# Optimization experiments

Measured on AMD Instinct MI355X. Metric: run time of the kernel, lower is better.

## Reference

```python
import jax, jax.numpy as jnp
from jax import lax
import numpy as np


def _fps(xyz, M):
    # Farthest point sampling: sequential over M steps, vectorized over batch.
    B, N, _ = xyz.shape
    def body(carry, _):
        dists, far = carry                       # dists:[B,N], far:[B]
        c = xyz[jnp.arange(B), far]              # [B,3] current centroid
        d = jnp.sum((xyz - c[:, None, :]) ** 2, axis=-1)
        dists = jnp.minimum(dists, d)
        nxt = jnp.argmax(dists, axis=-1).astype(jnp.int32)
        return (dists, nxt), far
    init = (jnp.full((B, N), 1e10, xyz.dtype), jnp.zeros((B,), jnp.int32))
    _, inds = lax.scan(body, init, None, length=M)
    return inds.T                                # [B, M]


def _ball_query(xyz, new_xyz, radius, K):
    # For each centroid pick first K point indices within radius; pad with first hit.
    N = xyz.shape[1]
    d2 = jnp.sum((new_xyz[:, :, None, :] - xyz[:, None, :, :]) ** 2, axis=-1)  # [B,M,N]
    ids = jnp.where(d2 <= radius * radius, jnp.arange(N)[None, None, :], N)
    ids = jnp.sort(ids, axis=-1)[..., :K]        # [B,M,K]
    return jnp.where(ids == N, ids[..., :1], ids)


_gather = jax.vmap(lambda p, i: p[i])            # p:[N,C], i:[M,K] -> [M,K,C]


def _mlp(x, layers):
    # Shared per-point MLP (1x1 conv + ReLU chain); BN omitted as in source head.
    for w, b in layers:
        x = jax.nn.relu(jnp.einsum('bmkc,cd->bmkd', x, w) + b)
    return x


def _sa(xyz, points, M, radius, K, layers):
    # Set-abstraction: FPS -> ball query -> group (centered xyz ++ feats) -> MLP -> max over K.
    fi = _fps(xyz, M)                                        # [B,M]
    new_xyz = jnp.take_along_axis(xyz, fi[..., None], axis=1)  # [B,M,3]
    gi = _ball_query(xyz, new_xyz, radius, K)                # [B,M,K]
    g_xyz = _gather(xyz, gi) - new_xyz[:, :, None, :]        # [B,M,K,3]
    g = jnp.concatenate([g_xyz, _gather(points, gi)], axis=-1)
    return new_xyz, jnp.max(_mlp(g, layers), axis=2)         # [B,M,Cout]


def _forward(xyz, points,
             w1a, b1a, w1b, b1b, w1c, b1c,
             w2a, b2a, w2b, b2b, w2c, b2c,
             w3a, b3a, w3b, b3b, w3c, b3c,
             lin1_w, lin2_w, cls_w, cls_b):
    B = xyz.shape[0]
    x1, f1 = _sa(xyz, points, 512, 0.2, 32, [(w1a, b1a), (w1b, b1b), (w1c, b1c)])
    x2, f2 = _sa(x1, f1, 128, 0.4, 64, [(w2a, b2a), (w2b, b2b), (w2c, b2c)])
    # group_all: single group containing all 128 points, feats = [xyz ++ points] (259 ch)
    g = jnp.concatenate([x2, f2], axis=-1)[:, None]           # [B,1,128,259]
    f3 = jnp.max(_mlp(g, [(w3a, b3a), (w3b, b3b), (w3c, b3c)]), axis=2)  # [B,1,1024]
    net = f3.reshape(B, -1)
    net = jax.nn.relu(net @ lin1_w)   # linear1 (no bias) + ReLU; dropout=identity (eval)
    net = jax.nn.relu(net @ lin2_w)
    return net @ cls_w + cls_b


def setup_inputs() -> dict:
    key = jax.random.key(0)
    ks = iter(jax.random.split(key, 40))
    B, N, NC = 32, 1024, 40
    inp = {}
    inp['xyz'] = jax.random.uniform(next(ks), (B, N, 3), jnp.float32, -1.0, 1.0)
    inp['points'] = jax.random.normal(next(ks), (B, N, 3), jnp.float32)
    def lin(cin, cout):
        w = jax.random.normal(next(ks), (cin, cout), jnp.float32) / np.float32(np.sqrt(cin))
        return w, jnp.zeros((cout,), jnp.float32)
    dims = {'1': [(6, 64), (64, 64), (64, 128)],
            '2': [(131, 128), (128, 128), (128, 256)],
            '3': [(259, 256), (256, 512), (512, 1024)]}
    for s, layer_dims in dims.items():
        for tag, (ci, co) in zip('abc', layer_dims):
            w, b = lin(ci, co)
            inp['w%s%s' % (s, tag)] = w
            inp['b%s%s' % (s, tag)] = b
    inp['lin1_w'] = jax.random.normal(next(ks), (1024, 512), jnp.float32) / np.float32(32.0)
    inp['lin2_w'] = jax.random.normal(next(ks), (512, 256), jnp.float32) / np.float32(np.sqrt(512))
    inp['cls_w'] = jax.random.normal(next(ks), (256, NC), jnp.float32) / np.float32(16.0)
    inp['cls_b'] = jnp.zeros((NC,), jnp.float32)
    return inp


def reference(xyz, points,
              w1a, b1a, w1b, b1b, w1c, b1c,
              w2a, b2a, w2b, b2b, w2c, b2c,
              w3a, b3a, w3b, b3b, w3c, b3c,
              lin1_w, lin2_w, cls_w, cls_b):
    return _forward(xyz, points,
                    w1a, b1a, w1b, b1b, w1c, b1c,
                    w2a, b2a, w2b, b2b, w2c, b2c,
                    w3a, b3a, w3b, b3b, w3c, b3c,
                    lin1_w, lin2_w, cls_w, cls_b)
```

## Files before the change

kernel.cpp:

```cpp
#include <hip/hip_runtime.h>

#define DEVFN __device__ __forceinline__

static inline int ceil_div(int a, int b) { return (a + b - 1) / b; }

typedef __attribute__((ext_vector_type(8))) short         bf16x8;
typedef __attribute__((ext_vector_type(4))) float         f32x4;
typedef __attribute__((ext_vector_type(8))) unsigned short u16x8;
typedef unsigned short us;

DEVFN us f2bf(float x) {
    unsigned u = __float_as_uint(x);
    unsigned r = ((u >> 16) & 1u) + 0x7fffu;
    return (us)((u + r) >> 16);
}
DEVFN float bf2f(us h) { return __uint_as_float(((unsigned)h) << 16); }

template<int CTRL>
DEVFN double dpp_max_step(double v)
{
    int lo = __double2loint(v), hi = __double2hiint(v);
    int tlo = __builtin_amdgcn_update_dpp(lo, lo, CTRL, 0xF, 0xF, false);
    int thi = __builtin_amdgcn_update_dpp(hi, hi, CTRL, 0xF, 0xF, false);
    return fmax(v, __hiloint2double(thi, tlo));
}

template<int N>
__global__ __launch_bounds__(64) void fps_kernel(const float* __restrict__ xyz, int M,
                                                 int* __restrict__ out_idx,
                                                 float* __restrict__ nxout)
{
    constexpr int PPL = N / 64;
    int b = blockIdx.x, lane = threadIdx.x;
    __shared__ float4 sp[N];
    const float* p = xyz + (size_t)b * N * 3;
    float px[PPL], py[PPL], pz[PPL], dd[PPL];
    unsigned lo[PPL];
    #pragma unroll
    for (int j = 0; j < PPL; ++j) {
        int idx = lane + 64 * j;
        px[j] = p[idx*3+0]; py[j] = p[idx*3+1]; pz[j] = p[idx*3+2];
        sp[idx] = make_float4(px[j], py[j], pz[j], 0.f);
        dd[j] = 1e10f;
        lo[j] = ~(unsigned)idx;
    }
    __syncthreads();
    int far = 0;
    for (int s = 0; s < M; ++s) {
        float4 c4 = sp[far];
        if (lane == 0) {
            out_idx[(size_t)b*M + s] = far;
            nxout[((size_t)b*M + s)*3 + 0] = c4.x;
            nxout[((size_t)b*M + s)*3 + 1] = c4.y;
            nxout[((size_t)b*M + s)*3 + 2] = c4.z;
        }
        double cand[PPL];
        #pragma unroll
        for (int j = 0; j < PPL; ++j) {
            float dx = __fsub_rn(px[j], c4.x);
            float dy = __fsub_rn(py[j], c4.y);
            float dz = __fsub_rn(pz[j], c4.z);
            float d  = __fadd_rn(__fadd_rn(__fmul_rn(dx,dx), __fmul_rn(dy,dy)),
                                 __fmul_rn(dz,dz));
            float nd = fminf(dd[j], d);
            dd[j] = nd;
            cand[j] = __hiloint2double(__float_as_int(nd), (int)lo[j]);
        }
        #pragma unroll
        for (int st = PPL/2; st > 0; st >>= 1)
            #pragma unroll
            for (int j = 0; j < PPL; ++j)
                if (j < st) cand[j] = fmax(cand[j], cand[j + st]);
        double v = cand[0];
        v = dpp_max_step<0xB1>(v);
        v = dpp_max_step<0x4E>(v);
        v = dpp_max_step<0x124>(v);
        v = dpp_max_step<0x128>(v);
        v = dpp_max_step<0x142>(v);
        v = dpp_max_step<0x143>(v);
        int wlo = __builtin_amdgcn_readlane(__double2loint(v), 63);
        far = (int)(~(unsigned)wlo);
    }
}

__global__ void ballquery_kernel(const float* __restrict__ xyz,
                                 const float* __restrict__ new_xyz,
                                 int* __restrict__ gi,
                                 int B, int N, int M, int K, float r2)
{
    int t = blockIdx.x * blockDim.x + threadIdx.x;
    if (t >= B * M) return;
    int b = t / M;
    const float* p = xyz + (size_t)b * N * 3;
    float cx = new_xyz[t*3+0], cy = new_xyz[t*3+1], cz = new_xyz[t*3+2];
    int* out = gi + (size_t)t * K;
    int cnt = 0, first = 0;
    bool havefirst = false;
    for (int i = 0; i < N; ++i) {
        float dx = __fsub_rn(p[i*3+0], cx);
        float dy = __fsub_rn(p[i*3+1], cy);
        float dz = __fsub_rn(p[i*3+2], cz);
        float d  = __fadd_rn(__fadd_rn(__fmul_rn(dx,dx), __fmul_rn(dy,dy)),
                             __fmul_rn(dz,dz));
        if (d <= r2) {
            if (!havefirst) { first = i; havefirst = true; }
            out[cnt++] = i;
            if (cnt == K) break;
        }
    }
    for (; cnt < K; ++cnt) out[cnt] = first;
}

DEVFN float f4_elem(const float4& v, int u) {
    return u == 0 ? v.x : u == 1 ? v.y : u == 2 ? v.z : v.w;
}

__global__ void wsplit_kernel(const float* __restrict__ w,
                              us* __restrict__ wh, us* __restrict__ wl,
                              int CItot, int CO, int CIpad, int ro)
{
    int t = blockIdx.x * 256 + threadIdx.x;
    if (t >= CIpad * CO) return;
    int co = t / CIpad, ci = t % CIpad;
    int src = ci + ro;
    float v = (src < CItot) ? w[(size_t)src * CO + co] : 0.f;
    us h = f2bf(v);
    wh[t] = h;
    wl[t] = f2bf(v - bf2f(h));
}

__global__ __launch_bounds__(256) void sa1_l1_fps2_kernel(
    const float* __restrict__ xyz, const float* __restrict__ feats,
    const float* __restrict__ new_xyz , const int* __restrict__ gi,
    const float* __restrict__ w, const float* __restrict__ bias,
    us* __restrict__ oh, us* __restrict__ ol,
    int row0, int nb_main, int fps_on,
    int* __restrict__ fps2, float* __restrict__ nx2)
{
    __shared__ float4 sp[512];
    if ((int)blockIdx.x >= nb_main) {
        if (!fps_on) return;
        constexpr int N = 512, PPL = 8, MS = 128;
        const int b   = blockIdx.x - nb_main;
        const int tid = threadIdx.x, lane = tid & 63;
        float px[PPL], py[PPL], pz[PPL], dd[PPL];
        unsigned lo[PPL];
        if (tid < 64) {
            const float* p = new_xyz + (size_t)b * N * 3;
            #pragma unroll
            for (int j = 0; j < PPL; ++j) {
                int idx = lane + 64 * j;
                px[j] = p[idx*3+0]; py[j] = p[idx*3+1]; pz[j] = p[idx*3+2];
                sp[idx] = make_float4(px[j], py[j], pz[j], 0.f);
                dd[j] = 1e10f;
                lo[j] = ~(unsigned)idx;
            }
        }
        __syncthreads();
        if (tid >= 64) return;
        int far = 0;
        for (int s = 0; s < MS; ++s) {
            float4 c4 = sp[far];
            if (lane == 0) {
                fps2[(size_t)b*MS + s] = far;
                nx2[((size_t)b*MS + s)*3 + 0] = c4.x;
                nx2[((size_t)b*MS + s)*3 + 1] = c4.y;
                nx2[((size_t)b*MS + s)*3 + 2] = c4.z;
            }
            double cand[PPL];
            #pragma unroll
            for (int j = 0; j < PPL; ++j) {
                float dx = __fsub_rn(px[j], c4.x);
                float dy = __fsub_rn(py[j], c4.y);
                float dz = __fsub_rn(pz[j], c4.z);
                float d  = __fadd_rn(__fadd_rn(__fmul_rn(dx,dx), __fmul_rn(dy,dy)),
                                     __fmul_rn(dz,dz));
                float nd = fminf(dd[j], d);
                dd[j] = nd;
                cand[j] = __hiloint2double(__float_as_int(nd), (int)lo[j]);
            }
            #pragma unroll
            for (int st = PPL/2; st > 0; st >>= 1)
                #pragma unroll
                for (int j = 0; j < PPL; ++j)
                    if (j < st) cand[j] = fmax(cand[j], cand[j + st]);
            double v = cand[0];
            v = dpp_max_step<0xB1>(v);
            v = dpp_max_step<0x4E>(v);
            v = dpp_max_step<0x124>(v);
            v = dpp_max_step<0x128>(v);
            v = dpp_max_step<0x142>(v);
            v = dpp_max_step<0x143>(v);
            int wlo = __builtin_amdgcn_readlane(__double2loint(v), 63);
            far = (int)(~(unsigned)wlo);
        }
        return;
    }
    constexpr int CF = 3, CO = 64, KPTS = 32, N = 1024, M = 512, WCH = 16;
    const int lane = threadIdx.x & 63;
    const int wv   = __builtin_amdgcn_readfirstlane(threadIdx.x >> 6);
    const int rl   = blockIdx.x * 64 + lane;
    const int row  = row0 + rl;
    const int cent = row / KPTS;
    const int b    = cent / M;
    const int idx  = gi[row];
    const float* pp  = xyz + ((size_t)b*N + idx)*3;
    const float* cc3 = new_xyz + (size_t)cent*3;
    float a0 = __fsub_rn(pp[0], cc3[0]);
    float a1 = __fsub_rn(pp[1], cc3[1]);
    float a2 = __fsub_rn(pp[2], cc3[2]);
    const float* frow = feats + ((size_t)b*N + idx)*CF;
    float f0 = frow[0], f1v = frow[1], f2v = frow[2];
    const float* wcol = w + wv*WCH;
    const float* bcol = bias + wv*WCH;
    float acc[WCH];
    #pragma unroll
    for (int j = 0; j < WCH; ++j) {
        float a = bcol[j];
        a += a0 * wcol[0*CO + j];
        a += a1 * wcol[1*CO + j];
        a += a2 * wcol[2*CO + j];
        a += f0 * wcol[3*CO + j];
        a += f1v * wcol[4*CO + j];
        a += f2v * wcol[5*CO + j];
        acc[j] = a;
    }
    #pragma unroll
    for (int j8 = 0; j8 < WCH; j8 += 8) {
        u16x8 hv, lv;
        #pragma unroll
        for (int u = 0; u < 8; ++u) {
            float v = fmaxf(acc[j8+u], 0.f);
            us h = f2bf(v);
            hv[u] = h;
            lv[u] = f2bf(v - bf2f(h));
        }
        size_t o = (size_t)rl*CO + wv*WCH + j8;
        *(u16x8*)(&oh[o]) = hv;
        *(u16x8*)(&ol[o]) = lv;
    }
}

__global__ __launch_bounds__(256) void sa1_l2_bq2_kernel(
    const us* __restrict__ ah, const us* __restrict__ al,
    const us* __restrict__ wh, const us* __restrict__ wl,
    const float* __restrict__ bias,
    us* __restrict__ oh, us* __restrict__ ol,
    int nb_main, int bq_on,
    const float* __restrict__ nx1, const float* __restrict__ nx2,
    int* __restrict__ gi2)
{
    if ((int)blockIdx.x >= nb_main) {
        if (!bq_on) return;
        int t = (blockIdx.x - nb_main) * 256 + threadIdx.x;
        if (t >= 32 * 128) return;
        constexpr int N = 512, M = 128, K = 64;
        const float r2 = (float)(0.4*0.4);
        int b = t / M;
        const float* p = nx1 + (size_t)b * N * 3;
        float cx = nx2[t*3+0], cy = nx2[t*3+1], cz = nx2[t*3+2];
        int* out = gi2 + (size_t)t * K;
        int cnt = 0, first = 0;
        bool havefirst = false;
        for (int i = 0; i < N; ++i) {
            float dx = __fsub_rn(p[i*3+0], cx);
            float dy = __fsub_rn(p[i*3+1], cy);
            float dz = __fsub_rn(p[i*3+2], cz);
            float d  = __fadd_rn(__fadd_rn(__fmul_rn(dx,dx), __fmul_rn(dy,dy)),
                                 __fmul_rn(dz,dz));
            if (d <= r2) {
                if (!havefirst) { first = i; havefirst = true; }
                out[cnt++] = i;
                if (cnt == K) break;
            }
        }
        for (; cnt < K; ++cnt) out[cnt] = first;
        return;
    }
    constexpr int CI = 64, CO = 64, KT = 2, NTILE = 4, MROW = 4;
    const int wid  = threadIdx.x >> 6;
    const int lane = threadIdx.x & 63;
    const int m    = lane & 15;
    const int kg   = lane >> 4;
    const int blockrow = blockIdx.x * (64 * MROW);
    bf16x8 Ahf[MROW * KT], Alf[MROW * KT];
    #pragma unroll
    for (int t = 0; t < MROW; ++t) {
        const us* arh = ah + (size_t)(blockrow + t*64 + wid*16 + m) * CI + kg * 8;
        const us* arl = al + (size_t)(blockrow + t*64 + wid*16 + m) * CI + kg * 8;
        #pragma unroll
        for (int kt = 0; kt < KT; ++kt) {
            Ahf[t*KT + kt] = *(const bf16x8*)(arh + kt*32);
            Alf[t*KT + kt] = *(const bf16x8*)(arl + kt*32);
        }
    }
    #pragma unroll
    for (int nt = 0; nt < NTILE; ++nt) {
        f32x4 acc[MROW];
        #pragma unroll
        for (int t = 0; t < MROW; ++t) acc[t] = (f32x4){0.f, 0.f, 0.f, 0.f};
        const us* wbh = wh + (size_t)(nt*16 + m) * CI + kg * 8;
        const us* wbl = wl + (size_t)(nt*16 + m) * CI + kg * 8;
        #pragma unroll
        for (int kt = 0; kt < KT; ++kt) {
            bf16x8 Bh = *(const bf16x8*)(wbh + kt*32);
            bf16x8 Bl = *(const bf16x8*)(wbl + kt*32);
            #pragma unroll
            for (int t = 0; t < MROW; ++t) {
                acc[t] = __builtin_amdgcn_mfma_f32_16x16x32_bf16(Ahf[t*KT+kt], Bh, acc[t], 0, 0, 0);
                acc[t] = __builtin_amdgcn_mfma_f32_16x16x32_bf16(Ahf[t*KT+kt], Bl, acc[t], 0, 0, 0);
                acc[t] = __builtin_amdgcn_mfma_f32_16x16x32_bf16(Alf[t*KT+kt], Bh, acc[t], 0, 0, 0);
            }
        }
        int dcol = nt*16 + m;
        float bv = bias[dcol];
        #pragma unroll
        for (int t = 0; t < MROW; ++t)
            #pragma unroll
            for (int r = 0; r < 4; ++r) {
                float v = fmaxf(acc[t][r] + bv, 0.f);
                size_t o = (size_t)(blockrow + t*64 + wid*16 + kg*4 + r) * CO + dcol;
                us h = f2bf(v);
                oh[o] = h;
                ol[o] = f2bf(v - bf2f(h));
            }
    }
}

template<int CI, int CO, int NTILE, int MROW, int KPTS, int OUTMODE>
__global__ __launch_bounds__(256) void mfma_layer_kernel(
    const us* __restrict__ ah, const us* __restrict__ al,
    const us* __restrict__ wh, const us* __restrict__ wl,
    const float* __restrict__ bias,
    us* __restrict__ oh, us* __restrict__ ol,
    float* __restrict__ ofp, int rowbase)
{
    constexpr int KT = CI / 32;
    static_assert(KT * MROW <= 18, "A-preload register budget");
    __shared__ float partial[4][OUTMODE >= 2 ? MROW : 1][OUTMODE >= 2 ? 16*NTILE : 1];
    const int wid  = threadIdx.x >> 6;
    const int lane = threadIdx.x & 63;
    const int m    = lane & 15;
    const int kg   = lane >> 4;
    const int blockrow = blockIdx.x * (64 * MROW);
    const int colbase  = blockIdx.y * (16 * NTILE);
    bf16x8 Ahf[MROW * KT], Alf[MROW * KT];
    #pragma unroll
    for (int t = 0; t < MROW; ++t) {
        const us* arh = ah + (size_t)(blockrow + t*64 + wid*16 + m) * CI + kg * 8;
        const us* arl = al + (size_t)(blockrow + t*64 + wid*16 + m) * CI + kg * 8;
        #pragma unroll
        for (int kt = 0; kt < KT; ++kt) {
            Ahf[t*KT + kt] = *(const bf16x8*)(arh + kt*32);
            Alf[t*KT + kt] = *(const bf16x8*)(arl + kt*32);
        }
    }
    #pragma unroll
    for (int nt = 0; nt < NTILE; ++nt) {
        f32x4 acc[MROW];
        #pragma unroll
        for (int t = 0; t < MROW; ++t) acc[t] = (f32x4){0.f, 0.f, 0.f, 0.f};
        const us* wbh = wh + (size_t)(colbase + nt*16 + m) * CI + kg * 8;
        const us* wbl = wl + (size_t)(colbase + nt*16 + m) * CI + kg * 8;
        #pragma unroll
        for (int kt = 0; kt < KT; ++kt) {
            bf16x8 Bh = *(const bf16x8*)(wbh + kt*32);
            bf16x8 Bl = *(const bf16x8*)(wbl + kt*32);
            #pragma unroll
            for (int t = 0; t < MROW; ++t) {
                acc[t] = __builtin_amdgcn_mfma_f32_16x16x32_bf16(Ahf[t*KT+kt], Bh, acc[t], 0, 0, 0);
                acc[t] = __builtin_amdgcn_mfma_f32_16x16x32_bf16(Ahf[t*KT+kt], Bl, acc[t], 0, 0, 0);
                acc[t] = __builtin_amdgcn_mfma_f32_16x16x32_bf16(Alf[t*KT+kt], Bh, acc[t], 0, 0, 0);
            }
        }
        int dcol = colbase + nt*16 + m;
        float bv = bias[dcol];
        #pragma unroll
        for (int t = 0; t < MROW; ++t) {
            float v[4];
            #pragma unroll
            for (int r = 0; r < 4; ++r) v[r] = fmaxf(acc[t][r] + bv, 0.f);
            if constexpr (OUTMODE == 0) {
                #pragma unroll
                for (int r = 0; r < 4; ++r) {
                    size_t o = (size_t)(blockrow + t*64 + wid*16 + kg*4 + r) * CO + dcol;
                    us h = f2bf(v[r]);
                    oh[o] = h;
                    ol[o] = f2bf(v[r] - bf2f(h));
                }
            } else if constexpr (OUTMODE == 1) {
                #pragma unroll
                for (int r = 0; r < 4; ++r)
                    ofp[(size_t)(blockrow + t*64 + wid*16 + kg*4 + r) * CO + dcol] = v[r];
            } else {
                float mx = fmaxf(fmaxf(v[0], v[1]), fmaxf(v[2], v[3]));
                mx = fmaxf(mx, __shfl_xor(mx, 16));
                mx = fmaxf(mx, __shfl_xor(mx, 32));
                if (lane < 16) partial[wid][t][nt*16 + m] = mx;
            }
        }
    }
    if constexpr (OUTMODE >= 2) {
        __syncthreads();
        for (int c = threadIdx.x; c < 16*NTILE; c += 256) {
            #pragma unroll
            for (int t = 0; t < MROW; ++t) {
                if constexpr (KPTS == 64) {
                    float mx = fmaxf(fmaxf(partial[0][t][c], partial[1][t][c]),
                                     fmaxf(partial[2][t][c], partial[3][t][c]));
                    int cent = (rowbase + blockrow) / 64 + t;
                    if constexpr (OUTMODE == 2) {
                        ofp[(size_t)cent*CO + colbase + c] = mx;
                    } else {
                        size_t o = (size_t)cent*CO + colbase + c;
                        us h = f2bf(mx);
                        oh[o] = h; ol[o] = f2bf(mx - bf2f(h));
                    }
                } else {
                    int cent0 = (rowbase + blockrow) / 32 + t*2;
                    float v0 = fmaxf(partial[0][t][c], partial[1][t][c]);
                    float v1 = fmaxf(partial[2][t][c], partial[3][t][c]);
                    if constexpr (OUTMODE == 2) {
                        ofp[(size_t)cent0*CO + colbase + c]     = v0;
                        ofp[(size_t)(cent0+1)*CO + colbase + c] = v1;
                    } else {
                        size_t o0 = (size_t)cent0*CO + colbase + c;
                        size_t o1 = (size_t)(cent0+1)*CO + colbase + c;
                        us h0 = f2bf(v0), h1 = f2bf(v1);
                        oh[o0] = h0; ol[o0] = f2bf(v0 - bf2f(h0));
                        oh[o1] = h1; ol[o1] = f2bf(v1 - bf2f(h1));
                    }
                }
            }
        }
    }
}

template<int NTILE, int MROW>
__global__ __launch_bounds__(256) void mfma_sa2l1_kernel(
    const float* __restrict__ sxyz, const float* __restrict__ cxyz,
    const int* __restrict__ gi,
    const us* __restrict__ f1h, const us* __restrict__ f1l,
    const float* __restrict__ w,
    const us* __restrict__ wh, const us* __restrict__ wl,
    const float* __restrict__ bias,
    us* __restrict__ oh, us* __restrict__ ol,
    int rowbase)
{
    constexpr int CI = 128, CO = 128, KT = 4, KPTS = 64, M = 128, N = 512;
    const int wid  = threadIdx.x >> 6;
    const int lane = threadIdx.x & 63;
    const int m    = lane & 15;
    const int kg   = lane >> 4;
    const int blockrow = blockIdx.x * (64 * MROW);
    const int colbase  = blockIdx.y * (16 * NTILE);
    bf16x8 Ahf[MROW * KT], Alf[MROW * KT];
    #pragma unroll
    for (int t = 0; t < MROW; ++t) {
        int grow = rowbase + blockrow + t*64 + wid*16 + m;
        int cent = grow / KPTS;
        int b    = cent / M;
        int idx  = gi[grow];
        const us* arh = f1h + ((size_t)b*N + idx) * CI + kg * 8;
        const us* arl = f1l + ((size_t)b*N + idx) * CI + kg * 8;
        #pragma unroll
        for (int kt = 0; kt < KT; ++kt) {
            Ahf[t*KT + kt] = *(const bf16x8*)(arh + kt*32);
            Alf[t*KT + kt] = *(const bf16x8*)(arl + kt*32);
        }
    }
    float dx[MROW][4], dy[MROW][4], dz[MROW][4];
    #pragma unroll
    for (int t = 0; t < MROW; ++t)
        #pragma unroll
        for (int r = 0; r < 4; ++r) {
            int grow = rowbase + blockrow + t*64 + wid*16 + kg*4 + r;
            int cent = grow / KPTS;
            int b    = cent / M;
            int idx  = gi[grow];
            const float* pp = sxyz + ((size_t)b*N + idx)*3;
            const float* cc = cxyz + (size_t)cent*3;
            dx[t][r] = __fsub_rn(pp[0], cc[0]);
            dy[t][r] = __fsub_rn(pp[1], cc[1]);
            dz[t][r] = __fsub_rn(pp[2], cc[2]);
        }
    #pragma unroll
    for (int nt = 0; nt < NTILE; ++nt) {
        f32x4 acc[MROW];
        #pragma unroll
        for (int t = 0; t < MROW; ++t) acc[t] = (f32x4){0.f, 0.f, 0.f, 0.f};
        const us* wbh = wh + (size_t)(colbase + nt*16 + m) * CI + kg * 8;
        const us* wbl = wl + (size_t)(colbase + nt*16 + m) * CI + kg * 8;
        #pragma unroll
        for (int kt = 0; kt < KT; ++kt) {
            bf16x8 Bh = *(const bf16x8*)(wbh + kt*32);
            bf16x8 Bl = *(const bf16x8*)(wbl + kt*32);
            #pragma unroll
            for (int t = 0; t < MROW; ++t) {
                acc[t] = __builtin_amdgcn_mfma_f32_16x16x32_bf16(Ahf[t*KT+kt], Bh, acc[t], 0, 0, 0);
                acc[t] = __builtin_amdgcn_mfma_f32_16x16x32_bf16(Ahf[t*KT+kt], Bl, acc[t], 0, 0, 0);
                acc[t] = __builtin_amdgcn_mfma_f32_16x16x32_bf16(Alf[t*KT+kt], Bh, acc[t], 0, 0, 0);
            }
        }
        int dcol = colbase + nt*16 + m;
        float w0 = w[0*CO + dcol], w1 = w[1*CO + dcol], w2 = w[2*CO + dcol];
        float bv = bias[dcol];
        #pragma unroll
        for (int t = 0; t < MROW; ++t)
            #pragma unroll
            for (int r = 0; r < 4; ++r) {
                float v = acc[t][r] + bv + dx[t][r]*w0 + dy[t][r]*w1 + dz[t][r]*w2;
                v = fmaxf(v, 0.f);
                size_t o = (size_t)(blockrow + t*64 + wid*16 + kg*4 + r) * CO + dcol;
                us h = f2bf(v);
                oh[o] = h;
                ol[o] = f2bf(v - bf2f(h));
            }
    }
}

__global__ void concat_split_kernel(const float* __restrict__ a, const float* __restrict__ f,
                                    us* __restrict__ oh, us* __restrict__ ol,
                                    int R, int CF, int CIpad)
{
    int t = blockIdx.x * 256 + threadIdx.x;
    if (t >= R * CIpad) return;
    int r = t / CIpad, c = t % CIpad;
    float v;
    if (c < 3) v = a[r*3 + c];
    else if (c < CF + 3) v = f[(size_t)r * CF + (c - 3)];
    else v = 0.f;
    us h = f2bf(v);
    oh[t] = h;
    ol[t] = f2bf(v - bf2f(h));
}

template<int RELU, int HASB>
__global__ __launch_bounds__(256) void fc_kernel(
    const float* __restrict__ A, const float* __restrict__ W,
    const float* __restrict__ bias, float* __restrict__ Cc,
    int Mr, int Nc, int Kd)
{
    int t = blockIdx.x * 256 + threadIdx.x;
    if (t >= Mr * Nc) return;
    int row = t / Nc, col = t % Nc;
    const float* a = A + (size_t)row * Kd;
    const float* w = W + col;
    float acc = 0.f;
    #pragma unroll 8
    for (int k = 0; k < Kd; ++k)
        acc += a[k] * w[(size_t)k * Nc];
    if (HASB) acc += bias[col];
    if (RELU) acc = fmaxf(acc, 0.f);
    Cc[t] = acc;
}

__global__ void rowmax_kernel(const float* __restrict__ in, float* __restrict__ out,
                              int B, int P, int C)
{
    int t = blockIdx.x * blockDim.x + threadIdx.x;
    if (t >= B * C) return;
    int b = t / C, c = t % C;
    const float* p = in + (size_t)b * P * C + c;
    float mx = p[0];
    for (int i = 1; i < P; ++i) mx = fmaxf(mx, p[(size_t)i * C]);
    out[t] = mx;
}

extern "C" void kernel_launch(void* const* d_in, const int* in_sizes, int n_in,
                              void* d_out, int out_size, void* d_ws, size_t ws_size,
                              hipStream_t stream)
{
    const float* xyz    = (const float*)d_in[0];
    const float* points = (const float*)d_in[1];
    const float* w1a = (const float*)d_in[2];  const float* b1a = (const float*)d_in[3];
    const float* w1b = (const float*)d_in[4];  const float* b1b = (const float*)d_in[5];
    const float* w1c = (const float*)d_in[6];  const float* b1c = (const float*)d_in[7];
    const float* w2a = (const float*)d_in[8];  const float* b2a = (const float*)d_in[9];
    const float* w2b = (const float*)d_in[10]; const float* b2b = (const float*)d_in[11];
    const float* w2c = (const float*)d_in[12]; const float* b2c = (const float*)d_in[13];
    const float* w3a = (const float*)d_in[14]; const float* b3a = (const float*)d_in[15];
    const float* w3b = (const float*)d_in[16]; const float* b3b = (const float*)d_in[17];
    const float* w3c = (const float*)d_in[18]; const float* b3c = (const float*)d_in[19];
    const float* lin1 = (const float*)d_in[20];
    const float* lin2 = (const float*)d_in[21];
    const float* clsw = (const float*)d_in[22];
    const float* clsb = (const float*)d_in[23];

    char* ws = (char*)d_ws;
    size_t off = 0;
    auto alloc = [&](size_t bytes) -> void* {
        void* p = ws + off;
        off += (bytes + 255) & ~(size_t)255;
        return p;
    };
    int*   fps1 = (int*)  alloc((size_t)32*512*4);
    float* nx1  = (float*)alloc((size_t)32*512*3*4);
    int*   gi1  = (int*)  alloc((size_t)32*512*32*4);
    int*   fps2 = (int*)  alloc((size_t)32*128*4);
    float* nx2  = (float*)alloc((size_t)32*128*3*4);
    int*   gi2  = (int*)  alloc((size_t)32*128*64*4);
    float* f2   = (float*)alloc((size_t)32*128*256*4);
    float* h3c  = (float*)alloc((size_t)4096*1024*4);
    float* f3   = (float*)alloc((size_t)32*1024*4);
    float* fc1  = (float*)alloc((size_t)32*512*4);
    float* fc2  = (float*)alloc((size_t)32*256*4);

    us* w1bh = (us*)alloc(64*64*2);     us* w1bl = (us*)alloc(64*64*2);
    us* w1ch = (us*)alloc(128*64*2);    us* w1cl = (us*)alloc(128*64*2);
    us* w2ah = (us*)alloc(128*128*2);   us* w2al = (us*)alloc(128*128*2);
    us* w2bh = (us*)alloc(128*128*2);   us* w2bl = (us*)alloc(128*128*2);
    us* w2ch = (us*)alloc(256*128*2);   us* w2cl = (us*)alloc(256*128*2);
    us* w3ah = (us*)alloc(256*288*2);   us* w3al = (us*)alloc(256*288*2);
    us* w3bh = (us*)alloc(512*256*2);   us* w3bl = (us*)alloc(512*256*2);
    us* w3ch = (us*)alloc(1024*512*2);  us* w3cl = (us*)alloc(1024*512*2);
    us* f1h  = (us*)alloc((size_t)16384*128*2);
    us* f1l  = (us*)alloc((size_t)16384*128*2);
    us* g3H  = (us*)alloc((size_t)4096*288*2);  us* g3L  = (us*)alloc((size_t)4096*288*2);
    us* h3aH = (us*)alloc((size_t)4096*256*2);  us* h3aL = (us*)alloc((size_t)4096*256*2);
    us* h3bH = (us*)alloc((size_t)4096*512*2);  us* h3bL = (us*)alloc((size_t)4096*512*2);

    size_t avail = (ws_size > off + 1024) ? (ws_size - off - 1024) : 0;
    size_t bufcap = avail / 4;
    if (bufcap > (size_t)67200000) bufcap = 67200000;
    us* Ah = (us*)alloc(bufcap); us* Al = (us*)alloc(bufcap);
    us* Bh = (us*)alloc(bufcap); us* Bl = (us*)alloc(bufcap);

    auto wsp = [&](const float* w, int CItot, int CO, int CIpad, int ro, us* wh, us* wl) {
        wsplit_kernel<<<ceil_div(CIpad*CO, 256), 256, 0, stream>>>(w, wh, wl, CItot, CO, CIpad, ro);
    };
    wsp(w1b, 64, 64, 64, 0,   w1bh, w1bl);
    wsp(w1c, 64, 128, 64, 0,  w1ch, w1cl);
    wsp(w2a, 131, 128, 128, 3, w2ah, w2al);
    wsp(w2b, 128, 128, 128, 0, w2bh, w2bl);
    wsp(w2c, 128, 256, 128, 0, w2ch, w2cl);
    wsp(w3a, 259, 256, 288, 0, w3ah, w3al);
    wsp(w3b, 256, 512, 256, 0, w3bh, w3bl);
    wsp(w3c, 512, 1024, 512, 0, w3ch, w3cl);

    fps_kernel<1024><<<32, 64, 0, stream>>>(xyz, 512, fps1, nx1);
    ballquery_kernel<<<ceil_div(32*512, 256), 256, 0, stream>>>(
        xyz, nx1, gi1, 32, 1024, 512, 32, (float)(0.2*0.2));
    {
        const int rows = 32*512*32;
        int ch = (int)((bufcap / (64*2)) & ~(size_t)1023);
        if (ch > rows) ch = rows;
        if (ch < 1024) ch = 1024;
        int first = 1;
        for (int r0 = 0; r0 < rows; r0 += ch) {
            int rc = rows - r0 < ch ? rows - r0 : ch;
            int nb1 = rc/64, nb2 = rc/256;
            sa1_l1_fps2_kernel<<<nb1 + (first ? 32 : 0), 256, 0, stream>>>(
                xyz, points, nx1, gi1, w1a, b1a, Ah, Al, r0, nb1, first, fps2, nx2);
            sa1_l2_bq2_kernel<<<nb2 + (first ? 16 : 0), 256, 0, stream>>>(
                Ah, Al, w1bh, w1bl, b1b, Bh, Bl, nb2, first, nx1, nx2, gi2);
            mfma_layer_kernel<64, 128, 8, 4, 32, 3><<<dim3(nb2, 1), 256, 0, stream>>>(
                Bh, Bl, w1ch, w1cl, b1c, f1h, f1l, nullptr, r0);
            first = 0;
        }
    }

    {
        const int rows = 32*128*64;
        int ch = (int)((bufcap / (128*2)) & ~(size_t)1023);
        if (ch > rows) ch = rows;
        if (ch < 1024) ch = 1024;
        for (int r0 = 0; r0 < rows; r0 += ch) {
            int rc = rows - r0 < ch ? rows - r0 : ch;
            mfma_sa2l1_kernel<8, 2><<<dim3(rc/128, 1), 256, 0, stream>>>(
                nx1, nx2, gi2, f1h, f1l, w2a, w2ah, w2al, b2a, Ah, Al, r0);
            mfma_layer_kernel<128, 128, 8, 4, 0, 0><<<dim3(rc/256, 1), 256, 0, stream>>>(
                Ah, Al, w2bh, w2bl, b2b, Bh, Bl, nullptr, 0);
            mfma_layer_kernel<128, 256, 16, 4, 64, 2><<<dim3(rc/256, 1), 256, 0, stream>>>(
                Bh, Bl, w2ch, w2cl, b2c, nullptr, nullptr, f2, r0);
        }
    }

    concat_split_kernel<<<ceil_div(4096*288, 256), 256, 0, stream>>>(
        nx2, f2, g3H, g3L, 4096, 256, 288);
    mfma_layer_kernel<288, 256, 2, 1, 0, 0><<<dim3(4096/64, 256/32), 256, 0, stream>>>(
        g3H, g3L, w3ah, w3al, b3a, h3aH, h3aL, nullptr, 0);
    mfma_layer_kernel<256, 512, 2, 2, 0, 0><<<dim3(4096/128, 512/32), 256, 0, stream>>>(
        h3aH, h3aL, w3bh, w3bl, b3b, h3bH, h3bL, nullptr, 0);
    mfma_layer_kernel<512, 1024, 4, 1, 0, 1><<<dim3(4096/64, 1024/64), 256, 0, stream>>>(
        h3bH, h3bL, w3ch, w3cl, b3c, nullptr, nullptr, h3c, 0);
    rowmax_kernel<<<ceil_div(32*1024, 256), 256, 0, stream>>>(h3c, f3, 32, 128, 1024);

    fc_kernel<1,0><<<ceil_div(32*512, 256), 256, 0, stream>>>(
        f3, lin1, nullptr, fc1, 32, 512, 1024);
    fc_kernel<1,0><<<ceil_div(32*256, 256), 256, 0, stream>>>(
        fc1, lin2, nullptr, fc2, 32, 256, 512);
    fc_kernel<0,1><<<ceil_div(32*40, 256), 256, 0, stream>>>(
        fc2, clsw, clsb, (float*)d_out, 32, 40, 256);
}
```

Before: 1.253 ms.

## Split farthest point sampling across four waves with LDS cross-wave argmax

The FPS loops now run on a 256-thread block instead of a single 64-lane wave, so each lane holds a quarter as many points. After the intra-wave DPP max, each wave writes its candidate to a double-buffered LDS slot and a block barrier lets all threads combine the four candidates. This cuts the per-step serial arithmetic on the latency-bound FPS chain, but adds a barrier and LDS round trip to every step. The second-stage FPS embedded in the fused kernel uses the same shared body.

```diff
diff --git a/kernel.cpp b/kernel.cpp
--- a/kernel.cpp
+++ b/kernel.cpp
@@ -26,19 +26,17 @@
 }
 
 template<int N>
-__global__ __launch_bounds__(64) void fps_kernel(const float* __restrict__ xyz, int M,
-                                                 int* __restrict__ out_idx,
-                                                 float* __restrict__ nxout)
-{
-    constexpr int PPL = N / 64;
-    int b = blockIdx.x, lane = threadIdx.x;
-    __shared__ float4 sp[N];
-    const float* p = xyz + (size_t)b * N * 3;
+DEVFN void fps4_body(const float* __restrict__ p, int MS,
+                     int* __restrict__ oidx, float* __restrict__ onx,
+                     float4* sp, double* kslots)
+{
+    constexpr int PPL = N / 256;
+    const int tid = threadIdx.x;
     float px[PPL], py[PPL], pz[PPL], dd[PPL];
     unsigned lo[PPL];
     #pragma unroll
     for (int j = 0; j < PPL; ++j) {
-        int idx = lane + 64 * j;
+        int idx = tid + 256 * j;
         px[j] = p[idx*3+0]; py[j] = p[idx*3+1]; pz[j] = p[idx*3+2];
         sp[idx] = make_float4(px[j], py[j], pz[j], 0.f);
         dd[j] = 1e10f;
@@ -46,13 +44,11 @@
     }
     __syncthreads();
     int far = 0;
-    for (int s = 0; s < M; ++s) {
+    for (int s = 0; s < MS; ++s) {
         float4 c4 = sp[far];
-        if (lane == 0) {
-            out_idx[(size_t)b*M + s] = far;
-            nxout[((size_t)b*M + s)*3 + 0] = c4.x;
-            nxout[((size_t)b*M + s)*3 + 1] = c4.y;
-            nxout[((size_t)b*M + s)*3 + 2] = c4.z;
+        if (tid == 0) {
+            oidx[s] = far;
+            onx[s*3+0] = c4.x; onx[s*3+1] = c4.y; onx[s*3+2] = c4.z;
         }
         double cand[PPL];
         #pragma unroll
@@ -78,9 +74,24 @@
         v = dpp_max_step<0x128>(v);
         v = dpp_max_step<0x142>(v);
         v = dpp_max_step<0x143>(v);
-        int wlo = __builtin_amdgcn_readlane(__double2loint(v), 63);
-        far = (int)(~(unsigned)wlo);
-    }
+        if ((tid & 63) == 63) kslots[(s & 1)*4 + (tid >> 6)] = v;
+        __syncthreads();
+        const double* ks = kslots + (s & 1)*4;
+        double kx = fmax(fmax(ks[0], ks[1]), fmax(ks[2], ks[3]));
+        far = (int)(~(unsigned)__double2loint(kx));
+    }
+}
+
+template<int N>
+__global__ __launch_bounds__(256) void fps4_kernel(const float* __restrict__ xyz, int M,
+                                                   int* __restrict__ out_idx,
+                                                   float* __restrict__ nxout)
+{
+    __shared__ float4 sp[N];
+    __shared__ double kslots[8];
+    int b = blockIdx.x;
+    fps4_body<N>(xyz + (size_t)b * N * 3, M,
+                 out_idx + (size_t)b * M, nxout + (size_t)b * M * 3, sp, kslots);
 }
 
 __global__ void ballquery_kernel(const float* __restrict__ xyz,
@@ -138,62 +149,13 @@
     int* __restrict__ fps2, float* __restrict__ nx2)
 {
     __shared__ float4 sp[512];
+    __shared__ double kslots[8];
     if ((int)blockIdx.x >= nb_main) {
         if (!fps_on) return;
-        constexpr int N = 512, PPL = 8, MS = 128;
-        const int b   = blockIdx.x - nb_main;
-        const int tid = threadIdx.x, lane = tid & 63;
-        float px[PPL], py[PPL], pz[PPL], dd[PPL];
-        unsigned lo[PPL];
-        if (tid < 64) {
-            const float* p = new_xyz + (size_t)b * N * 3;
-            #pragma unroll
-            for (int j = 0; j < PPL; ++j) {
-                int idx = lane + 64 * j;
-                px[j] = p[idx*3+0]; py[j] = p[idx*3+1]; pz[j] = p[idx*3+2];
-                sp[idx] = make_float4(px[j], py[j], pz[j], 0.f);
-                dd[j] = 1e10f;
-                lo[j] = ~(unsigned)idx;
-            }
-        }
-        __syncthreads();
-        if (tid >= 64) return;
-        int far = 0;
-        for (int s = 0; s < MS; ++s) {
-            float4 c4 = sp[far];
-            if (lane == 0) {
-                fps2[(size_t)b*MS + s] = far;
-                nx2[((size_t)b*MS + s)*3 + 0] = c4.x;
-                nx2[((size_t)b*MS + s)*3 + 1] = c4.y;
-                nx2[((size_t)b*MS + s)*3 + 2] = c4.z;
-            }
-            double cand[PPL];
-            #pragma unroll
-            for (int j = 0; j < PPL; ++j) {
-                float dx = __fsub_rn(px[j], c4.x);
-                float dy = __fsub_rn(py[j], c4.y);
-                float dz = __fsub_rn(pz[j], c4.z);
-                float d  = __fadd_rn(__fadd_rn(__fmul_rn(dx,dx), __fmul_rn(dy,dy)),
-                                     __fmul_rn(dz,dz));
-                float nd = fminf(dd[j], d);
-                dd[j] = nd;
-                cand[j] = __hiloint2double(__float_as_int(nd), (int)lo[j]);
-            }
-            #pragma unroll
-            for (int st = PPL/2; st > 0; st >>= 1)
-                #pragma unroll
-                for (int j = 0; j < PPL; ++j)
-                    if (j < st) cand[j] = fmax(cand[j], cand[j + st]);
-            double v = cand[0];
-            v = dpp_max_step<0xB1>(v);
-            v = dpp_max_step<0x4E>(v);
-            v = dpp_max_step<0x124>(v);
-            v = dpp_max_step<0x128>(v);
-            v = dpp_max_step<0x142>(v);
-            v = dpp_max_step<0x143>(v);
-            int wlo = __builtin_amdgcn_readlane(__double2loint(v), 63);
-            far = (int)(~(unsigned)wlo);
-        }
+        const int b = blockIdx.x - nb_main;
+        fps4_body<512>(new_xyz + (size_t)b * 512 * 3, 128,
+                       fps2 + (size_t)b * 128, nx2 + (size_t)b * 128 * 3,
+                       sp, kslots);
         return;
     }
     constexpr int CF = 3, CO = 64, KPTS = 32, N = 1024, M = 512, WCH = 16;
@@ -638,7 +600,7 @@
     wsp(w3b, 256, 512, 256, 0, w3bh, w3bl);
     wsp(w3c, 512, 1024, 512, 0, w3ch, w3cl);
 
-    fps_kernel<1024><<<32, 64, 0, stream>>>(xyz, 512, fps1, nx1);
+    fps4_kernel<1024><<<32, 256, 0, stream>>>(xyz, 512, fps1, nx1);
     ballquery_kernel<<<ceil_div(32*512, 256), 256, 0, stream>>>(
         xyz, nx1, gi1, 32, 1024, 512, 32, (float)(0.2*0.2));
     {
```

Result: faster. 1.225 ms (-2.3%).
